# Kernel optimization log

Hardware: AMD Instinct MI355X
Metric: run time of the kernel (lower is better)

## Reference

```python
import jax, jax.numpy as jnp
import numpy as np
from jax import lax

DEPTH = 2
PATCH_SIZE = 16
PATCH_SIZE_FINAL = PATCH_SIZE // (2 ** DEPTH)  # 4
NUM_CHANNELS = 3
NUM_PATCHES = 196
NUM_PATCHES_FINAL = NUM_PATCHES * (4 ** DEPTH)  # 3136
EMB_DIM = NUM_CHANNELS * PATCH_SIZE_FINAL ** 2  # 48


def patchify(X, p):
    # X: [B, C, H, W] -> [B, (H//p)*(W//p), C, p, p], patches in row-major order
    B, C, H, W = X.shape
    eh, ew = H // p, W // p
    x = X.reshape(B, C, eh, p, ew, p)
    x = x.transpose(0, 2, 4, 1, 3, 5)  # [B, eh, ew, C, p, p]
    return x.reshape(B, eh * ew, C, p, p)


def unpatchify(x):
    # x: [B, n, C, p, p] with n = e*e -> [B, 1, C, e*p, e*p]
    B, n, C, p, _ = x.shape
    e = int(np.sqrt(n))
    img = x.reshape(B, e, e, C, p, p).transpose(0, 3, 1, 4, 2, 5).reshape(B, C, e * p, e * p)
    return img[:, None]  # [B, 1, C, H, W]


def conv_same(X, W, b):
    # NCHW conv with 3x3 kernel, 'same' padding
    y = lax.conv_general_dilated(X, W, window_strides=(1, 1), padding='SAME',
                                 dimension_numbers=('NCHW', 'OIHW', 'NCHW'))
    return y + b[None, :, None, None]


def setup_inputs() -> dict:
    key = jax.random.key(0)
    k1, k2, k3, k4 = jax.random.split(key, 4)
    return {
        'X': jax.random.normal(k1, (128, 3, 224, 224), dtype=jnp.float32),
        'conv_w': jax.random.normal(k2, (3, 3, 3, 3), dtype=jnp.float32) * 0.1,
        'conv_b': jax.random.normal(k3, (3,), dtype=jnp.float32) * 0.1,
        'pos_emb': jax.random.normal(k4, (NUM_PATCHES_FINAL, EMB_DIM), dtype=jnp.float32),
    }


def reference(X, conv_w, conv_b, pos_emb):
    B = X.shape[0]
    X = conv_same(X, conv_w, conv_b)
    # patch at fine granularity and add learned position embeddings
    pat = patchify(X, PATCH_SIZE_FINAL)                      # [B, 3136, 3, 4, 4]
    flat = pat.reshape(B, NUM_PATCHES_FINAL, EMB_DIM) + pos_emb[None]
    # unflatten + unpatch back to full image
    enc = flat.reshape(B, NUM_PATCHES_FINAL, NUM_CHANNELS, PATCH_SIZE_FINAL, PATCH_SIZE_FINAL)
    img = unpatchify(enc)                                    # [B, 1, 3, 224, 224]
    # re-patch at coarse granularity (patch() squeezes the singleton dim)
    out = patchify(img[:, 0], PATCH_SIZE)                    # [B, 196, 3, 16, 16]
    return out.reshape(B, NUM_PATCHES, NUM_CHANNELS * PATCH_SIZE ** 2)
```

## Files before the change

### kernel.cpp

```cpp
#include <hip/hip_runtime.h>

#define HW 224
#define CHW (HW*HW)
#define ROWS_PER_WAVE 7

__global__ __launch_bounds__(256) void patch_conv_kernel(
    const float* __restrict__ X,
    const float* __restrict__ Wt,
    const float* __restrict__ Bv,
    const float* __restrict__ P,
    float* __restrict__ out)
{
    const int b    = blockIdx.y;
    const int tid  = threadIdx.x;
    const int lane = tid & 63;
    const int wv   = tid >> 6;
    const int strip = blockIdx.x * 4 + wv;
    const int r0   = strip * ROWS_PER_WAVE;
    const int x0   = lane * 4;
    const bool act = (x0 < HW);

    float w[3][3][3][3];
    #pragma unroll
    for (int i = 0; i < 81; ++i)
        ((float*)w)[i] = Wt[i];
    const float b0 = Bv[0], b1 = Bv[1], b2 = Bv[2];

    const float* Xb = X + (size_t)b * (3 * CHW);

    float e[3][3][6];

    auto load_row = [&](int ci, int y, float* dst) {
        float4 v = make_float4(0.f, 0.f, 0.f, 0.f);
        if ((unsigned)y < HW && act)
            v = *(const float4*)(Xb + ci * CHW + y * HW + x0);
        float l  = __shfl_up(v.w, 1);
        float rr = __shfl_down(v.x, 1);
        if (lane == 0) l = 0.f;
        if (x0 + 4 >= HW) rr = 0.f;
        dst[0] = l; dst[1] = v.x; dst[2] = v.y; dst[3] = v.z; dst[4] = v.w; dst[5] = rr;
    };

    #pragma unroll
    for (int ci = 0; ci < 3; ++ci) {
        load_row(ci, r0 - 1, e[ci][0]);
        load_row(ci, r0,     e[ci][1]);
        load_row(ci, r0 + 1, e[ci][2]);
    }

    const int nc_col = x0 >> 4;
    const int xl     = x0 & 15;
    const int nf_col = x0 >> 2;

    float* ob = out + (size_t)b * (196 * 768);

    #pragma unroll
    for (int i = 0; i < ROWS_PER_WAVE; ++i) {
        const int y   = r0 + i;
        const int sm1 = i % 3, s0 = (i + 1) % 3, sp1 = (i + 2) % 3;

        float acc[3][4];
        #pragma unroll
        for (int co = 0; co < 3; ++co)
            #pragma unroll
            for (int j = 0; j < 4; ++j) acc[co][j] = 0.f;

        #pragma unroll
        for (int ci = 0; ci < 3; ++ci) {
            const float* rows[3] = { e[ci][sm1], e[ci][s0], e[ci][sp1] };
            #pragma unroll
            for (int kh = 0; kh < 3; ++kh) {
                const float* rr = rows[kh];
                #pragma unroll
                for (int co = 0; co < 3; ++co) {
                    const float w0 = w[co][ci][kh][0];
                    const float w1 = w[co][ci][kh][1];
                    const float w2 = w[co][ci][kh][2];
                    #pragma unroll
                    for (int j = 0; j < 4; ++j)
                        acc[co][j] += w0 * rr[j] + w1 * rr[j + 1] + w2 * rr[j + 2];
                }
            }
        }

        #pragma unroll
        for (int ci = 0; ci < 3; ++ci)
            load_row(ci, y + 2, e[ci][sm1]);

        if (act) {
            const int nf  = (y >> 2) * 56 + nf_col;
            const int sub = (y & 3) * 4;
            const int nc  = (y >> 4) * 14 + nc_col;
            float* op = ob + nc * 768 + (y & 15) * 16 + xl;

            const float4 p0 = *(const float4*)(P + nf * 48 + 0 * 16 + sub);
            const float4 p1 = *(const float4*)(P + nf * 48 + 1 * 16 + sub);
            const float4 p2 = *(const float4*)(P + nf * 48 + 2 * 16 + sub);

            *(float4*)(op + 0)   = make_float4(acc[0][0] + b0 + p0.x, acc[0][1] + b0 + p0.y,
                                               acc[0][2] + b0 + p0.z, acc[0][3] + b0 + p0.w);
            *(float4*)(op + 256) = make_float4(acc[1][0] + b1 + p1.x, acc[1][1] + b1 + p1.y,
                                               acc[1][2] + b1 + p1.z, acc[1][3] + b1 + p1.w);
            *(float4*)(op + 512) = make_float4(acc[2][0] + b2 + p2.x, acc[2][1] + b2 + p2.y,
                                               acc[2][2] + b2 + p2.z, acc[2][3] + b2 + p2.w);
        }
    }
}

extern "C" void kernel_launch(void* const* d_in, const int* in_sizes, int n_in,
                              void* d_out, int out_size, void* d_ws, size_t ws_size,
                              hipStream_t stream) {
    const float* X  = (const float*)d_in[0];
    const float* Wt = (const float*)d_in[1];
    const float* Bv = (const float*)d_in[2];
    const float* P  = (const float*)d_in[3];
    float* out = (float*)d_out;

    dim3 grid(8, 128);
    patch_conv_kernel<<<grid, 256, 0, stream>>>(X, Wt, Bv, P, out);
}
```

Baseline: 47.54 us.

## Compute one output row per wave instead of a seven-row rolling strip

New measurement: 48.94 us. 1.03x slower.

```diff
diff --git a/kernel.cpp b/kernel.cpp
--- a/kernel.cpp
+++ b/kernel.cpp
@@ -2,7 +2,6 @@
 
 #define HW 224
 #define CHW (HW*HW)
-#define ROWS_PER_WAVE 7
 
 __global__ __launch_bounds__(256) void patch_conv_kernel(
     const float* __restrict__ X,
@@ -11,100 +10,63 @@
     const float* __restrict__ P,
     float* __restrict__ out)
 {
-    const int b    = blockIdx.y;
     const int tid  = threadIdx.x;
     const int lane = tid & 63;
     const int wv   = tid >> 6;
-    const int strip = blockIdx.x * 4 + wv;
-    const int r0   = strip * ROWS_PER_WAVE;
+    const int y    = blockIdx.x * 4 + wv;
+    const int b    = blockIdx.y;
     const int x0   = lane * 4;
-    const bool act = (x0 < HW);
+    if (x0 >= HW) return;
 
-    float w[3][3][3][3];
+    float w[81];
     #pragma unroll
-    for (int i = 0; i < 81; ++i)
-        ((float*)w)[i] = Wt[i];
-    const float b0 = Bv[0], b1 = Bv[1], b2 = Bv[2];
+    for (int i = 0; i < 81; ++i) w[i] = Wt[i];
 
     const float* Xb = X + (size_t)b * (3 * CHW);
 
-    float e[3][3][6];
-
-    auto load_row = [&](int ci, int y, float* dst) {
-        float4 v = make_float4(0.f, 0.f, 0.f, 0.f);
-        if ((unsigned)y < HW && act)
-            v = *(const float4*)(Xb + ci * CHW + y * HW + x0);
-        float l  = __shfl_up(v.w, 1);
-        float rr = __shfl_down(v.x, 1);
-        if (lane == 0) l = 0.f;
-        if (x0 + 4 >= HW) rr = 0.f;
-        dst[0] = l; dst[1] = v.x; dst[2] = v.y; dst[3] = v.z; dst[4] = v.w; dst[5] = rr;
-    };
+    const int nf  = (y >> 2) * 56 + (x0 >> 2);
+    const int sub = (y & 3) * 4;
+    float acc[3][4];
+    #pragma unroll
+    for (int co = 0; co < 3; ++co) {
+        const float4 p = *(const float4*)(P + nf * 48 + co * 16 + sub);
+        const float bb = Bv[co];
+        acc[co][0] = bb + p.x; acc[co][1] = bb + p.y;
+        acc[co][2] = bb + p.z; acc[co][3] = bb + p.w;
+    }
 
     #pragma unroll
     for (int ci = 0; ci < 3; ++ci) {
-        load_row(ci, r0 - 1, e[ci][0]);
-        load_row(ci, r0,     e[ci][1]);
-        load_row(ci, r0 + 1, e[ci][2]);
+        const float* Xc = Xb + ci * CHW;
+        #pragma unroll
+        for (int ky = 0; ky < 3; ++ky) {
+            const int ry = y - 1 + ky;
+            float rr[6];
+            if ((unsigned)ry < HW) {
+                const float* row = Xc + ry * HW;
+                const float4 v = *(const float4*)(row + x0);
+                rr[1] = v.x; rr[2] = v.y; rr[3] = v.z; rr[4] = v.w;
+                rr[0] = (x0 > 0)      ? row[x0 - 1] : 0.f;
+                rr[5] = (x0 + 4 < HW) ? row[x0 + 4] : 0.f;
+            } else {
+                rr[0] = rr[1] = rr[2] = rr[3] = rr[4] = rr[5] = 0.f;
+            }
+            #pragma unroll
+            for (int co = 0; co < 3; ++co) {
+                const float* wp = w + (co * 3 + ci) * 9 + ky * 3;
+                #pragma unroll
+                for (int j = 0; j < 4; ++j)
+                    acc[co][j] += wp[0] * rr[j] + wp[1] * rr[j + 1] + wp[2] * rr[j + 2];
+            }
+        }
     }
 
-    const int nc_col = x0 >> 4;
-    const int xl     = x0 & 15;
-    const int nf_col = x0 >> 2;
-
-    float* ob = out + (size_t)b * (196 * 768);
-
+    const int nc = (y >> 4) * 14 + (x0 >> 4);
+    float* op = out + (size_t)b * (196 * 768) + nc * 768 + (y & 15) * 16 + (x0 & 15);
     #pragma unroll
-    for (int i = 0; i < ROWS_PER_WAVE; ++i) {
-        const int y   = r0 + i;
-        const int sm1 = i % 3, s0 = (i + 1) % 3, sp1 = (i + 2) % 3;
-
-        float acc[3][4];
-        #pragma unroll
-        for (int co = 0; co < 3; ++co)
-            #pragma unroll
-            for (int j = 0; j < 4; ++j) acc[co][j] = 0.f;
-
-        #pragma unroll
-        for (int ci = 0; ci < 3; ++ci) {
-            const float* rows[3] = { e[ci][sm1], e[ci][s0], e[ci][sp1] };
-            #pragma unroll
-            for (int kh = 0; kh < 3; ++kh) {
-                const float* rr = rows[kh];
-                #pragma unroll
-                for (int co = 0; co < 3; ++co) {
-                    const float w0 = w[co][ci][kh][0];
-                    const float w1 = w[co][ci][kh][1];
-                    const float w2 = w[co][ci][kh][2];
-                    #pragma unroll
-                    for (int j = 0; j < 4; ++j)
-                        acc[co][j] += w0 * rr[j] + w1 * rr[j + 1] + w2 * rr[j + 2];
-                }
-            }
-        }
-
-        #pragma unroll
-        for (int ci = 0; ci < 3; ++ci)
-            load_row(ci, y + 2, e[ci][sm1]);
-
-        if (act) {
-            const int nf  = (y >> 2) * 56 + nf_col;
-            const int sub = (y & 3) * 4;
-            const int nc  = (y >> 4) * 14 + nc_col;
-            float* op = ob + nc * 768 + (y & 15) * 16 + xl;
-
-            const float4 p0 = *(const float4*)(P + nf * 48 + 0 * 16 + sub);
-            const float4 p1 = *(const float4*)(P + nf * 48 + 1 * 16 + sub);
-            const float4 p2 = *(const float4*)(P + nf * 48 + 2 * 16 + sub);
-
-            *(float4*)(op + 0)   = make_float4(acc[0][0] + b0 + p0.x, acc[0][1] + b0 + p0.y,
-                                               acc[0][2] + b0 + p0.z, acc[0][3] + b0 + p0.w);
-            *(float4*)(op + 256) = make_float4(acc[1][0] + b1 + p1.x, acc[1][1] + b1 + p1.y,
-                                               acc[1][2] + b1 + p1.z, acc[1][3] + b1 + p1.w);
-            *(float4*)(op + 512) = make_float4(acc[2][0] + b2 + p2.x, acc[2][1] + b2 + p2.y,
-                                               acc[2][2] + b2 + p2.z, acc[2][3] + b2 + p2.w);
-        }
-    }
+    for (int co = 0; co < 3; ++co)
+        *(float4*)(op + co * 256) =
+            make_float4(acc[co][0], acc[co][1], acc[co][2], acc[co][3]);
 }
 
 extern "C" void kernel_launch(void* const* d_in, const int* in_sizes, int n_in,
@@ -116,6 +78,6 @@
     const float* P  = (const float*)d_in[3];
     float* out = (float*)d_out;
 
-    dim3 grid(8, 128);
+    dim3 grid(56, 128);
     patch_conv_kernel<<<grid, 256, 0, stream>>>(X, Wt, Bv, P, out);
 }
```
